# Kernel tuning notes

Hardware: AMD Instinct MI355X
Metric: run time of the kernel (lower is better)

The kernel has to match this reference:

```python
import jax, jax.numpy as jnp
import numpy as np

N_NODES = 40000
N_EDGES = 320000
IN_C = 256
OUT_C = 256
K = 5


def setup_inputs() -> dict:
    key = jax.random.key(0)
    k1, k2, k3, k4, k5 = jax.random.split(key, 5)
    x = jax.random.normal(k1, (N_NODES, IN_C), dtype=jnp.float32)
    edge_index = jax.random.randint(k2, (2, N_EDGES), 0, N_NODES, dtype=jnp.int64)
    edge_weight = jax.random.uniform(k3, (N_EDGES,), dtype=jnp.float32)
    # parameters: uniform(-stdv, stdv) with stdv = 1/sqrt(in_channels * K)
    stdv = 1.0 / np.sqrt(IN_C * K)
    weight = jax.random.uniform(k4, (K, IN_C, OUT_C), dtype=jnp.float32,
                                minval=-stdv, maxval=stdv)
    bias = jax.random.uniform(k5, (OUT_C,), dtype=jnp.float32,
                              minval=-stdv, maxval=stdv)
    return {"x": x, "edge_index": edge_index, "edge_weight": edge_weight,
            "weight": weight, "bias": bias}


def reference(x, edge_index, edge_weight, weight, bias):
    row, col = edge_index[0], edge_index[1]
    num_nodes = x.shape[0]
    k_order = weight.shape[0]

    # remove_self_loops: mask out row==col edges (static-shape equivalent)
    keep = (row != col)
    ew = jnp.where(keep, edge_weight, 0.0)

    # degree over rows (counting only non-self-loop edges), D^{-1/2}
    deg = jax.ops.segment_sum(keep.astype(x.dtype), row, num_segments=num_nodes)
    deg_inv_sqrt = jnp.where(deg > 0, jax.lax.rsqrt(jnp.maximum(deg, 1.0)), 0.0)

    # scaled Laplacian edge values: -d_r^{-1/2} * w * d_c^{-1/2}
    lap = -deg_inv_sqrt[row] * ew * deg_inv_sqrt[col]

    def spmm(v):  # [N, C] -> [N, C] : scatter-add of lap-weighted gathered rows
        return jax.ops.segment_sum(lap[:, None] * v[col], row, num_segments=num_nodes)

    # Chebyshev recursion: T0 = x, T1 = L x, T_k = 2 L T_{k-1} - T_{k-2}
    tx0 = x
    out = tx0 @ weight[0]
    if k_order > 1:
        tx1 = spmm(x)
        out = out + tx1 @ weight[1]
        for k in range(2, k_order):
            tx2 = 2.0 * spmm(tx1) - tx0
            out = out + tx2 @ weight[k]
            tx0, tx1 = tx1, tx2
    return out + bias
```

## Files before the change

kernel.cpp:

```cpp
#include <hip/hip_runtime.h>

#define NN 40000
#define NE 320000
#define C 256
#define KORD 5
#define KT 1280

typedef __attribute__((ext_vector_type(8))) short short8;
typedef __attribute__((ext_vector_type(4))) float floatx4;
typedef unsigned short bf16_t;

__device__ __forceinline__ bf16_t f2bf(float f) {
    union { float f; unsigned u; } v; v.f = f;
    unsigned r = v.u + 0x7fffu + ((v.u >> 16) & 1u);
    return (bf16_t)(r >> 16);
}
__device__ __forceinline__ float bf2f(bf16_t h) {
    union { unsigned u; float f; } v; v.u = ((unsigned)h) << 16;
    return v.f;
}

#define GLL16(gsrc, ldst)                                                        \
    __builtin_amdgcn_global_load_lds(                                            \
        (const __attribute__((address_space(1))) void*)(gsrc),                   \
        (__attribute__((address_space(3))) void*)(ldst), 16, 0, 0)


__global__ void count_kernel(const int* __restrict__ ei,
                             int* __restrict__ deg_keep,
                             int* __restrict__ cnt_all) {
    int e = blockIdx.x * 256 + threadIdx.x;
    if (e >= NE) return;
    int r = ei[e];
    int c = ei[NE + e];
    atomicAdd(&cnt_all[r], 1);
    if (r != c) atomicAdd(&deg_keep[r], 1);
}

__global__ void dis_kernel(const int* __restrict__ deg, float* __restrict__ dis) {
    int n = blockIdx.x * 256 + threadIdx.x;
    if (n >= NN) return;
    int d = deg[n];
    dis[n] = (d > 0) ? rsqrtf((float)d) : 0.0f;
}

__global__ void scan1_kernel(const int* __restrict__ cnt,
                             int* __restrict__ incl,
                             int* __restrict__ bsum) {
    __shared__ int s[256];
    int t = threadIdx.x;
    int idx = blockIdx.x * 256 + t;
    int v = (idx < NN) ? cnt[idx] : 0;
    s[t] = v;
    __syncthreads();
    for (int off = 1; off < 256; off <<= 1) {
        int add = (t >= off) ? s[t - off] : 0;
        __syncthreads();
        s[t] += add;
        __syncthreads();
    }
    if (idx < NN) incl[idx] = s[t];
    if (t == 255) bsum[blockIdx.x] = s[255];
}

__global__ void scan2_kernel(int* __restrict__ bsum, int nb) {
    __shared__ int s[256];
    int t = threadIdx.x;
    int v = (t < nb) ? bsum[t] : 0;
    s[t] = v;
    __syncthreads();
    for (int off = 1; off < 256; off <<= 1) {
        int add = (t >= off) ? s[t - off] : 0;
        __syncthreads();
        s[t] += add;
        __syncthreads();
    }
    if (t < nb) bsum[t] = s[t] - v;
}

__global__ void scan3_kernel(const int* __restrict__ cnt,
                             const int* __restrict__ incl,
                             const int* __restrict__ bexcl,
                             int* __restrict__ row_ptr,
                             int* __restrict__ cursor) {
    int idx = blockIdx.x * 256 + threadIdx.x;
    if (idx == 0) row_ptr[NN] = NE;
    if (idx >= NN) return;
    int rp = incl[idx] - cnt[idx] + bexcl[blockIdx.x];
    row_ptr[idx] = rp;
    cursor[idx]  = rp;
}

__global__ void fill_kernel(const int* __restrict__ ei,
                            const float* __restrict__ ew,
                            const float* __restrict__ dis,
                            int* __restrict__ cursor,
                            int* __restrict__ csr_col,
                            float* __restrict__ csr_val) {
    int e = blockIdx.x * 256 + threadIdx.x;
    if (e >= NE) return;
    int r = ei[e];
    int c = ei[NE + e];
    int pos = atomicAdd(&cursor[r], 1);
    float w = (r != c) ? ew[e] : 0.0f;
    csr_col[pos] = c;
    csr_val[pos] = -dis[r] * w * dis[c];
}

__global__ void convx_kernel(const float* __restrict__ x, bf16_t* __restrict__ abf) {
    int i = blockIdx.x * 256 + threadIdx.x;
    if (i >= NN * 64) return;
    int n = i >> 6, cg = i & 63;
    float4 f = *(const float4*)&x[(size_t)n * C + cg * 4];
    ushort4 h;
    h.x = f2bf(f.x); h.y = f2bf(f.y); h.z = f2bf(f.z); h.w = f2bf(f.w);
    *(ushort4*)&abf[(size_t)n * KT + cg * 4] = h;
}

__global__ void wt_kernel(const float* __restrict__ W, bf16_t* __restrict__ WT) {
    int t = blockIdx.x * 256 + threadIdx.x;
    if (t >= 256 * KT) return;
    int n = t & 255, kt = t >> 8;
    WT[(size_t)n * KT + kt] = f2bf(W[(size_t)kt * 256 + n]);
}

__global__ __launch_bounds__(256)
void spmm_kernel(const bf16_t* __restrict__ Vb,
                 const bf16_t* __restrict__ subb,
                 const int* __restrict__ row_ptr,
                 const int* __restrict__ csr_col,
                 const float* __restrict__ csr_val,
                 bf16_t* __restrict__ outb,
                 float alpha, int use_sub) {
    int wave = __builtin_amdgcn_readfirstlane(threadIdx.x >> 6);
    int lane = threadIdx.x & 63;
    int n = blockIdx.x * 4 + wave;
    int j0 = row_ptr[n];
    int j1 = row_ptr[n + 1];
    int cb = lane * 4;
    float a0 = 0.f, a1 = 0.f, a2 = 0.f, a3 = 0.f;
    int j = j0;
    for (; j + 8 <= j1; j += 8) {
        int cc[8]; float ww[8]; ushort4 vv[8];
#pragma unroll
        for (int u = 0; u < 8; ++u) { cc[u] = csr_col[j + u]; ww[u] = csr_val[j + u]; }
#pragma unroll
        for (int u = 0; u < 8; ++u) vv[u] = *(const ushort4*)&Vb[(size_t)cc[u] * KT + cb];
#pragma unroll
        for (int u = 0; u < 8; ++u) {
            a0 += ww[u] * bf2f(vv[u].x); a1 += ww[u] * bf2f(vv[u].y);
            a2 += ww[u] * bf2f(vv[u].z); a3 += ww[u] * bf2f(vv[u].w);
        }
    }
    for (; j + 4 <= j1; j += 4) {
        int cc[4]; float ww[4]; ushort4 vv[4];
#pragma unroll
        for (int u = 0; u < 4; ++u) { cc[u] = csr_col[j + u]; ww[u] = csr_val[j + u]; }
#pragma unroll
        for (int u = 0; u < 4; ++u) vv[u] = *(const ushort4*)&Vb[(size_t)cc[u] * KT + cb];
#pragma unroll
        for (int u = 0; u < 4; ++u) {
            a0 += ww[u] * bf2f(vv[u].x); a1 += ww[u] * bf2f(vv[u].y);
            a2 += ww[u] * bf2f(vv[u].z); a3 += ww[u] * bf2f(vv[u].w);
        }
    }
    for (; j < j1; ++j) {
        int   col = csr_col[j];
        float w   = csr_val[j];
        ushort4 v = *(const ushort4*)&Vb[(size_t)col * KT + cb];
        a0 += w * bf2f(v.x); a1 += w * bf2f(v.y);
        a2 += w * bf2f(v.z); a3 += w * bf2f(v.w);
    }
    float r0, r1, r2, r3;
    if (use_sub) {
        ushort4 s = *(const ushort4*)&subb[(size_t)n * KT + cb];
        r0 = alpha * a0 - bf2f(s.x);
        r1 = alpha * a1 - bf2f(s.y);
        r2 = alpha * a2 - bf2f(s.z);
        r3 = alpha * a3 - bf2f(s.w);
    } else {
        r0 = alpha * a0; r1 = alpha * a1; r2 = alpha * a2; r3 = alpha * a3;
    }
    ushort4 h;
    h.x = f2bf(r0); h.y = f2bf(r1); h.z = f2bf(r2); h.w = f2bf(r3);
    *(ushort4*)&outb[(size_t)n * KT + cb] = h;
}

__global__ __launch_bounds__(256, 5)
void gemm_mfma(const bf16_t* __restrict__ Abf,
               const bf16_t* __restrict__ WT,
               const float* __restrict__ bias,
               float* __restrict__ out) {
    __shared__ bf16_t smem[12288];
    int tid = threadIdx.x;
    int w = tid >> 6, lane = tid & 63;
    int m0 = blockIdx.x * 64;
    int n0 = blockIdx.y * 128;
    int wm = w & 1, wn = w >> 1;
    int quad = lane >> 4, l16 = lane & 15, l7 = l16 & 7;

    const bf16_t* srcbase[6];
#pragma unroll
    for (int j = 0; j < 6; ++j) {
        int gi = (w * 6 + j) * 64 + lane;
        int isB = gi >= 512;
        int t  = isB ? gi - 512 : gi;
        int row = t >> 3;
        int pg = t & 7;
        int g  = pg ^ (row & 7);
        srcbase[j] = (isB ? WT + (size_t)(n0 + row) * KT
                          : Abf + (size_t)(m0 + row) * KT) + g * 8;
    }

    int arowb = wm * 32 + l16;
    int browb = wn * 64 + l16;

    floatx4 acc[2][4] = {};

    for (int k0 = 0; k0 < KT; k0 += 64) {
        __syncthreads();
#pragma unroll
        for (int j = 0; j < 6; ++j)
            GLL16(srcbase[j] + k0, &smem[(w * 6 + j) * 512]);
        __syncthreads();

#pragma unroll
        for (int c = 0; c < 2; ++c) {
            int gp   = (c * 4 + quad) ^ l7;
            int aoff = (arowb * 8 + gp) * 8;
            int boff = 4096 + (browb * 8 + gp) * 8;
            short8 af[2], bfr[4];
#pragma unroll
            for (int mt = 0; mt < 2; ++mt) af[mt]  = *(const short8*)&smem[aoff + mt * 1024];
#pragma unroll
            for (int nt = 0; nt < 4; ++nt) bfr[nt] = *(const short8*)&smem[boff + nt * 1024];
#pragma unroll
            for (int mt = 0; mt < 2; ++mt)
#pragma unroll
                for (int nt = 0; nt < 4; ++nt)
                    acc[mt][nt] = __builtin_amdgcn_mfma_f32_16x16x32_bf16(
                        af[mt], bfr[nt], acc[mt][nt], 0, 0, 0);
        }
    }

#pragma unroll
    for (int nt = 0; nt < 4; ++nt) {
        int n = n0 + wn * 64 + nt * 16 + l16;
        float bv = bias[n];
#pragma unroll
        for (int mt = 0; mt < 2; ++mt) {
            int mbase = m0 + wm * 32 + mt * 16 + quad * 4;
#pragma unroll
            for (int r = 0; r < 4; ++r)
                out[(size_t)(mbase + r) * C + n] = acc[mt][nt][r] + bv;
        }
    }
}


extern "C" void kernel_launch(void* const* d_in, const int* in_sizes, int n_in,
                              void* d_out, int out_size, void* d_ws, size_t ws_size,
                              hipStream_t stream) {
    const float* x    = (const float*)d_in[0];
    const int*   ei   = (const int*)d_in[1];
    const float* ew   = (const float*)d_in[2];
    const float* W    = (const float*)d_in[3];
    const float* bias = (const float*)d_in[4];
    float* out = (float*)d_out;

    char* p = (char*)d_ws;
    auto carve = [&](size_t bytes) {
        char* q = p;
        p += (bytes + 255) & ~(size_t)255;
        return q;
    };
    int*    deg     = (int*)   carve(NN * 4);
    int*    cnt     = (int*)   carve(NN * 4);
    int*    incl    = (int*)   carve(NN * 4);
    int*    bsum    = (int*)   carve(256 * 4);
    int*    row_ptr = (int*)   carve((NN + 1) * 4);
    int*    cursor  = (int*)   carve(NN * 4);
    int*    csr_col = (int*)   carve(NE * 4);
    float*  csr_val = (float*) carve(NE * 4);
    float*  dis     = (float*) carve(NN * 4);
    bf16_t* abf     = (bf16_t*)carve((size_t)NN * KT * 2);
    bf16_t* WT      = (bf16_t*)carve((size_t)C * KT * 2);
    (void)ws_size; (void)n_in; (void)in_sizes; (void)out_size;

    const int NB_E = (NE + 255) / 256;
    const int NB_N = (NN + 255) / 256;

    hipMemsetAsync(deg, 0, NN * 4, stream);
    hipMemsetAsync(cnt, 0, NN * 4, stream);

    count_kernel<<<NB_E, 256, 0, stream>>>(ei, deg, cnt);
    dis_kernel<<<NB_N, 256, 0, stream>>>(deg, dis);
    scan1_kernel<<<NB_N, 256, 0, stream>>>(cnt, incl, bsum);
    scan2_kernel<<<1, 256, 0, stream>>>(bsum, NB_N);
    scan3_kernel<<<NB_N, 256, 0, stream>>>(cnt, incl, bsum, row_ptr, cursor);
    fill_kernel<<<NB_E, 256, 0, stream>>>(ei, ew, dis, cursor, csr_col, csr_val);

    convx_kernel<<<(NN * 64 + 255) / 256, 256, 0, stream>>>(x, abf);
    wt_kernel<<<(256 * KT + 255) / 256, 256, 0, stream>>>(W, WT);

    spmm_kernel<<<NN / 4, 256, 0, stream>>>(abf + 0 * 256, nullptr, row_ptr, csr_col,
                                            csr_val, abf + 1 * 256, 1.0f, 0);
    spmm_kernel<<<NN / 4, 256, 0, stream>>>(abf + 1 * 256, abf + 0 * 256, row_ptr,
                                            csr_col, csr_val, abf + 2 * 256, 2.0f, 1);
    spmm_kernel<<<NN / 4, 256, 0, stream>>>(abf + 2 * 256, abf + 1 * 256, row_ptr,
                                            csr_col, csr_val, abf + 3 * 256, 2.0f, 1);
    spmm_kernel<<<NN / 4, 256, 0, stream>>>(abf + 3 * 256, abf + 2 * 256, row_ptr,
                                            csr_col, csr_val, abf + 4 * 256, 2.0f, 1);

    dim3 ggrid(625, 2);
    gemm_mfma<<<ggrid, 256, 0, stream>>>(abf, WT, bias, out);
}
```

Measured before the change: 307.2 us.

## Widen SpMM gathers to 16B per lane, tile weight transpose, fuse dis into fill

The SpMM kernel now handles 16 rows per block. Each wave processes 4 rows, with the two half-waves gathering alternate edges as 16-byte loads and combining them through a cross-half shuffle, so fewer, wider memory transactions are issued. The weight transpose goes through an LDS tile so that both its reads and writes are coalesced. The separate rsqrt-degree kernel is removed and its computation is inlined into fill_kernel, which saves one launch at the cost of redundant rsqrt work per edge. Each row still runs a serial edge loop, and every row now issues half as many gather instructions.

Measured after the change: 322.1 us. 4.9% more time.

```diff
diff --git a/kernel.cpp b/kernel.cpp
--- a/kernel.cpp
+++ b/kernel.cpp
@@ -35,13 +35,6 @@
     int c = ei[NE + e];
     atomicAdd(&cnt_all[r], 1);
     if (r != c) atomicAdd(&deg_keep[r], 1);
-}
-
-__global__ void dis_kernel(const int* __restrict__ deg, float* __restrict__ dis) {
-    int n = blockIdx.x * 256 + threadIdx.x;
-    if (n >= NN) return;
-    int d = deg[n];
-    dis[n] = (d > 0) ? rsqrtf((float)d) : 0.0f;
 }
 
 __global__ void scan1_kernel(const int* __restrict__ cnt,
@@ -93,7 +86,7 @@
 
 __global__ void fill_kernel(const int* __restrict__ ei,
                             const float* __restrict__ ew,
-                            const float* __restrict__ dis,
+                            const int* __restrict__ deg,
                             int* __restrict__ cursor,
                             int* __restrict__ csr_col,
                             float* __restrict__ csr_val) {
@@ -103,8 +96,11 @@
     int c = ei[NE + e];
     int pos = atomicAdd(&cursor[r], 1);
     float w = (r != c) ? ew[e] : 0.0f;
+    int dr = deg[r], dc = deg[c];
+    float fr = (dr > 0) ? rsqrtf((float)dr) : 0.0f;
+    float fc = (dc > 0) ? rsqrtf((float)dc) : 0.0f;
     csr_col[pos] = c;
-    csr_val[pos] = -dis[r] * w * dis[c];
+    csr_val[pos] = -fr * w * fc;
 }
 
 __global__ void convx_kernel(const float* __restrict__ x, bf16_t* __restrict__ abf) {
@@ -118,10 +114,21 @@
 }
 
 __global__ void wt_kernel(const float* __restrict__ W, bf16_t* __restrict__ WT) {
-    int t = blockIdx.x * 256 + threadIdx.x;
-    if (t >= 256 * KT) return;
-    int n = t & 255, kt = t >> 8;
-    WT[(size_t)n * KT + kt] = f2bf(W[(size_t)kt * 256 + n]);
+    __shared__ float tile[64][65];
+    int k0 = blockIdx.x * 64;
+    int n0 = blockIdx.y * 64;
+    int tx = threadIdx.x & 63, ty = threadIdx.x >> 6;
+#pragma unroll
+    for (int i = 0; i < 16; ++i) {
+        int k = ty * 16 + i;
+        tile[k][tx] = W[(size_t)(k0 + k) * 256 + n0 + tx];
+    }
+    __syncthreads();
+#pragma unroll
+    for (int i = 0; i < 16; ++i) {
+        int n = ty * 16 + i;
+        WT[(size_t)(n0 + n) * KT + k0 + tx] = f2bf(tile[tx][n]);
+    }
 }
 
 __global__ __launch_bounds__(256)
@@ -132,58 +139,70 @@
                  const float* __restrict__ csr_val,
                  bf16_t* __restrict__ outb,
                  float alpha, int use_sub) {
-    int wave = __builtin_amdgcn_readfirstlane(threadIdx.x >> 6);
-    int lane = threadIdx.x & 63;
-    int n = blockIdx.x * 4 + wave;
-    int j0 = row_ptr[n];
-    int j1 = row_ptr[n + 1];
-    int cb = lane * 4;
-    float a0 = 0.f, a1 = 0.f, a2 = 0.f, a3 = 0.f;
-    int j = j0;
-    for (; j + 8 <= j1; j += 8) {
-        int cc[8]; float ww[8]; ushort4 vv[8];
-#pragma unroll
-        for (int u = 0; u < 8; ++u) { cc[u] = csr_col[j + u]; ww[u] = csr_val[j + u]; }
-#pragma unroll
-        for (int u = 0; u < 8; ++u) vv[u] = *(const ushort4*)&Vb[(size_t)cc[u] * KT + cb];
-#pragma unroll
-        for (int u = 0; u < 8; ++u) {
-            a0 += ww[u] * bf2f(vv[u].x); a1 += ww[u] * bf2f(vv[u].y);
-            a2 += ww[u] * bf2f(vv[u].z); a3 += ww[u] * bf2f(vv[u].w);
-        }
-    }
-    for (; j + 4 <= j1; j += 4) {
-        int cc[4]; float ww[4]; ushort4 vv[4];
-#pragma unroll
-        for (int u = 0; u < 4; ++u) { cc[u] = csr_col[j + u]; ww[u] = csr_val[j + u]; }
-#pragma unroll
-        for (int u = 0; u < 4; ++u) vv[u] = *(const ushort4*)&Vb[(size_t)cc[u] * KT + cb];
-#pragma unroll
-        for (int u = 0; u < 4; ++u) {
-            a0 += ww[u] * bf2f(vv[u].x); a1 += ww[u] * bf2f(vv[u].y);
-            a2 += ww[u] * bf2f(vv[u].z); a3 += ww[u] * bf2f(vv[u].w);
-        }
-    }
-    for (; j < j1; ++j) {
-        int   col = csr_col[j];
-        float w   = csr_val[j];
-        ushort4 v = *(const ushort4*)&Vb[(size_t)col * KT + cb];
-        a0 += w * bf2f(v.x); a1 += w * bf2f(v.y);
-        a2 += w * bf2f(v.z); a3 += w * bf2f(v.w);
-    }
-    float r0, r1, r2, r3;
-    if (use_sub) {
-        ushort4 s = *(const ushort4*)&subb[(size_t)n * KT + cb];
-        r0 = alpha * a0 - bf2f(s.x);
-        r1 = alpha * a1 - bf2f(s.y);
-        r2 = alpha * a2 - bf2f(s.z);
-        r3 = alpha * a3 - bf2f(s.w);
-    } else {
-        r0 = alpha * a0; r1 = alpha * a1; r2 = alpha * a2; r3 = alpha * a3;
-    }
-    ushort4 h;
-    h.x = f2bf(r0); h.y = f2bf(r1); h.z = f2bf(r2); h.w = f2bf(r3);
-    *(ushort4*)&outb[(size_t)n * KT + cb] = h;
+    __shared__ int rp[17];
+    int tid = threadIdx.x;
+    int n0 = blockIdx.x * 16;
+    if (tid < 17) rp[tid] = row_ptr[n0 + tid];
+    __syncthreads();
+    int wave = tid >> 6;
+    int lane = tid & 63;
+    int half = lane >> 5;
+    int l32  = lane & 31;
+    int ce   = l32 * 8;
+
+#pragma unroll
+    for (int i = 0; i < 4; ++i) {
+        int local = wave * 4 + i;
+        int n  = n0 + local;
+        int j0 = rp[local], j1 = rp[local + 1];
+        float acc[8] = {0, 0, 0, 0, 0, 0, 0, 0};
+        int j = j0;
+        for (; j + 4 <= j1; j += 4) {
+            int   e0 = j + half,     e1 = j + 2 + half;
+            int   c0 = csr_col[e0],  c1 = csr_col[e1];
+            float w0 = csr_val[e0],  w1 = csr_val[e1];
+            uint4 v0 = *(const uint4*)&Vb[(size_t)c0 * KT + ce];
+            uint4 v1 = *(const uint4*)&Vb[(size_t)c1 * KT + ce];
+            const bf16_t* p0 = (const bf16_t*)&v0;
+            const bf16_t* p1 = (const bf16_t*)&v1;
+#pragma unroll
+            for (int k = 0; k < 8; ++k)
+                acc[k] += w0 * bf2f(p0[k]) + w1 * bf2f(p1[k]);
+        }
+        if (j + 2 <= j1) {
+            int   e = j + half;
+            int   c = csr_col[e];
+            float w = csr_val[e];
+            uint4 v = *(const uint4*)&Vb[(size_t)c * KT + ce];
+            const bf16_t* pv = (const bf16_t*)&v;
+#pragma unroll
+            for (int k = 0; k < 8; ++k) acc[k] += w * bf2f(pv[k]);
+            j += 2;
+        }
+        if (j < j1) {
+            int   c = csr_col[j];
+            float w = half ? 0.0f : csr_val[j];
+            uint4 v = *(const uint4*)&Vb[(size_t)c * KT + ce];
+            const bf16_t* pv = (const bf16_t*)&v;
+#pragma unroll
+            for (int k = 0; k < 8; ++k) acc[k] += w * bf2f(pv[k]);
+        }
+#pragma unroll
+        for (int k = 0; k < 8; ++k) acc[k] += __shfl_xor(acc[k], 32);
+        if (half == 0) {
+            union { ushort us[8]; uint4 v; } r;
+            if (use_sub) {
+                uint4 sv = *(const uint4*)&subb[(size_t)n * KT + ce];
+                const bf16_t* ps = (const bf16_t*)&sv;
+#pragma unroll
+                for (int k = 0; k < 8; ++k) r.us[k] = f2bf(alpha * acc[k] - bf2f(ps[k]));
+            } else {
+#pragma unroll
+                for (int k = 0; k < 8; ++k) r.us[k] = f2bf(alpha * acc[k]);
+            }
+            *(uint4*)&outb[(size_t)n * KT + ce] = r.v;
+        }
+    }
 }
 
 __global__ __launch_bounds__(256, 5)
@@ -282,7 +301,6 @@
     int*    cursor  = (int*)   carve(NN * 4);
     int*    csr_col = (int*)   carve(NE * 4);
     float*  csr_val = (float*) carve(NE * 4);
-    float*  dis     = (float*) carve(NN * 4);
     bf16_t* abf     = (bf16_t*)carve((size_t)NN * KT * 2);
     bf16_t* WT      = (bf16_t*)carve((size_t)C * KT * 2);
     (void)ws_size; (void)n_in; (void)in_sizes; (void)out_size;
@@ -294,23 +312,25 @@
     hipMemsetAsync(cnt, 0, NN * 4, stream);
 
     count_kernel<<<NB_E, 256, 0, stream>>>(ei, deg, cnt);
-    dis_kernel<<<NB_N, 256, 0, stream>>>(deg, dis);
     scan1_kernel<<<NB_N, 256, 0, stream>>>(cnt, incl, bsum);
     scan2_kernel<<<1, 256, 0, stream>>>(bsum, NB_N);
     scan3_kernel<<<NB_N, 256, 0, stream>>>(cnt, incl, bsum, row_ptr, cursor);
-    fill_kernel<<<NB_E, 256, 0, stream>>>(ei, ew, dis, cursor, csr_col, csr_val);
+    fill_kernel<<<NB_E, 256, 0, stream>>>(ei, ew, deg, cursor, csr_col, csr_val);
 
     convx_kernel<<<(NN * 64 + 255) / 256, 256, 0, stream>>>(x, abf);
-    wt_kernel<<<(256 * KT + 255) / 256, 256, 0, stream>>>(W, WT);
-
-    spmm_kernel<<<NN / 4, 256, 0, stream>>>(abf + 0 * 256, nullptr, row_ptr, csr_col,
-                                            csr_val, abf + 1 * 256, 1.0f, 0);
-    spmm_kernel<<<NN / 4, 256, 0, stream>>>(abf + 1 * 256, abf + 0 * 256, row_ptr,
-                                            csr_col, csr_val, abf + 2 * 256, 2.0f, 1);
-    spmm_kernel<<<NN / 4, 256, 0, stream>>>(abf + 2 * 256, abf + 1 * 256, row_ptr,
-                                            csr_col, csr_val, abf + 3 * 256, 2.0f, 1);
-    spmm_kernel<<<NN / 4, 256, 0, stream>>>(abf + 3 * 256, abf + 2 * 256, row_ptr,
-                                            csr_col, csr_val, abf + 4 * 256, 2.0f, 1);
+    {
+        dim3 tg(20, 4);
+        wt_kernel<<<tg, 256, 0, stream>>>(W, WT);
+    }
+
+    spmm_kernel<<<NN / 16, 256, 0, stream>>>(abf + 0 * 256, nullptr, row_ptr, csr_col,
+                                             csr_val, abf + 1 * 256, 1.0f, 0);
+    spmm_kernel<<<NN / 16, 256, 0, stream>>>(abf + 1 * 256, abf + 0 * 256, row_ptr,
+                                             csr_col, csr_val, abf + 2 * 256, 2.0f, 1);
+    spmm_kernel<<<NN / 16, 256, 0, stream>>>(abf + 2 * 256, abf + 1 * 256, row_ptr,
+                                             csr_col, csr_val, abf + 3 * 256, 2.0f, 1);
+    spmm_kernel<<<NN / 16, 256, 0, stream>>>(abf + 3 * 256, abf + 2 * 256, row_ptr,
+                                             csr_col, csr_val, abf + 4 * 256, 2.0f, 1);
 
     dim3 ggrid(625, 2);
     gemm_mfma<<<ggrid, 256, 0, stream>>>(abf, WT, bias, out);
```
